# Kernel tuning notes

Measured on AMD Instinct MI355X. Metric: run time of the kernel, lower is better.

The kernel has to match this reference:

```python
import jax, jax.numpy as jnp
import numpy as np


def _procrustes_align(X, Y):
    """Batched similarity-transform (scipy-style Procrustes, reflection allowed).
    Aligns Y (pred) to X (target). X, Y: [B, N, 3]. Returns aligned Y: [B, N, 3].
    """
    muX = X.mean(axis=1, keepdims=True)                      # [B,1,3]
    muY = Y.mean(axis=1, keepdims=True)
    X0 = X - muX
    Y0 = Y - muY
    normX = jnp.sqrt((X0 ** 2).sum(axis=(1, 2), keepdims=True))  # [B,1,1]
    normY = jnp.sqrt((Y0 ** 2).sum(axis=(1, 2), keepdims=True))
    X0n = X0 / normX
    Y0n = Y0 / normY
    # 3x3 cross-covariance per batch element
    M = jnp.einsum('bni,bnj->bij', X0n, Y0n)                 # [B,3,3]
    U, s, Vt = jnp.linalg.svd(M)                             # batched tiny SVD
    # Optimal rotation Q = V @ U^T = (U @ Vt)^T  (minimizes ||Y0n @ Q - X0n||)
    Q = jnp.swapaxes(jnp.matmul(U, Vt), -1, -2)              # [B,3,3]
    traceTA = s.sum(-1)[:, None, None]                       # [B,1,1]
    Z = normX * traceTA * jnp.einsum('bni,bij->bnj', Y0n, Q) + muX
    return Z


def setup_inputs() -> dict:
    key = jax.random.key(0)
    k1, k2 = jax.random.split(key)
    B, N = 262144, 21
    pred_kp3d = jax.random.normal(k1, (B, N, 3), dtype=jnp.float32)
    target_kp3d = jax.random.normal(k2, (B, N, 3), dtype=jnp.float32)
    return {"pred_kp3d": pred_kp3d, "target_kp3d": target_kp3d}


def reference(pred_kp3d, target_kp3d):
    pred_aligned = _procrustes_align(target_kp3d, pred_kp3d)
    # mean per-joint Euclidean distance (PA-MPJPE style)
    err = jnp.sqrt(((pred_aligned - target_kp3d) ** 2).sum(-1)).mean()
    return err
```

## Files before the change

### kernel.cpp

```cpp
#include <hip/hip_runtime.h>
#include <math.h>

#define NPTS 21
#define FLB  63

__global__ __launch_bounds__(64, 2)
void pa_mpjpe(const float* __restrict__ pred,
              const float* __restrict__ targ,
              float* __restrict__ ws,
              int B)
{
    const int b = blockIdx.x * 64 + threadIdx.x;
    float errsum = 0.0f;

    if (b < B) {
        const float* gp = pred + (size_t)b * FLB;
        const float* gt = targ + (size_t)b * FLB;

        float yv[FLB];
        float xv[FLB];
        #pragma unroll
        for (int i = 0; i < 15; ++i) __builtin_memcpy(&yv[4*i], gp + 4*i, 16);
        __builtin_memcpy(&yv[60], gp + 60, 12);
        #pragma unroll
        for (int i = 0; i < 15; ++i) __builtin_memcpy(&xv[4*i], gt + 4*i, 16);
        __builtin_memcpy(&xv[60], gt + 60, 12);

        float sy0 = 0.f, sy1 = 0.f, sy2 = 0.f, syy = 0.f;
        #pragma unroll
        for (int n = 0; n < NPTS; ++n) {
            float a = yv[3*n+0], bb = yv[3*n+1], d = yv[3*n+2];
            sy0 += a; sy1 += bb; sy2 += d;
            syy = fmaf(a, a, fmaf(bb, bb, fmaf(d, d, syy)));
        }

        float sx0 = 0.f, sx1 = 0.f, sx2 = 0.f;
        float m00=0,m01=0,m02=0, m10=0,m11=0,m12=0, m20=0,m21=0,m22=0;
        #pragma unroll
        for (int n = 0; n < NPTS; ++n) {
            float a = xv[3*n+0], bb = xv[3*n+1], d = xv[3*n+2];
            float u = yv[3*n+0], v = yv[3*n+1], w = yv[3*n+2];
            sx0 += a; sx1 += bb; sx2 += d;
            m00 = fmaf(a,u,m00); m01 = fmaf(a,v,m01); m02 = fmaf(a,w,m02);
            m10 = fmaf(bb,u,m10); m11 = fmaf(bb,v,m11); m12 = fmaf(bb,w,m12);
            m20 = fmaf(d,u,m20); m21 = fmaf(d,v,m21); m22 = fmaf(d,w,m22);
        }

        const float invN = 1.0f / (float)NPTS;
        float mux0 = sx0*invN, mux1 = sx1*invN, mux2 = sx2*invN;
        float muy0 = sy0*invN, muy1 = sy1*invN, muy2 = sy2*invN;
        float ny2  = syy - (sy0*sy0 + sy1*sy1 + sy2*sy2) * invN;
        float c00 = m00 - sx0*sy0*invN, c01 = m01 - sx0*sy1*invN, c02 = m02 - sx0*sy2*invN;
        float c10 = m10 - sx1*sy0*invN, c11 = m11 - sx1*sy1*invN, c12 = m12 - sx1*sy2*invN;
        float c20 = m20 - sx2*sy0*invN, c21 = m21 - sx2*sy1*invN, c22 = m22 - sx2*sy2*invN;

        float q00=c00, q01=c10, q02=c20,
              q10=c01, q11=c11, q12=c21,
              q20=c02, q21=c12, q22=c22;
        #pragma unroll
        for (int it = 0; it < 8; ++it) {
            float C00 = q11*q22 - q12*q21;
            float C01 = q12*q20 - q10*q22;
            float C02 = q10*q21 - q11*q20;
            float C10 = q02*q21 - q01*q22;
            float C11 = q00*q22 - q02*q20;
            float C12 = q01*q20 - q00*q21;
            float C20 = q01*q12 - q02*q11;
            float C21 = q02*q10 - q00*q12;
            float C22 = q00*q11 - q01*q10;
            float det = q00*C00 + q01*C01 + q02*C02;
            float ad  = fmaxf(fabsf(det), 1e-30f);
            float sdet = copysignf(ad, det);
            float g  = __expf(0.333333333f * __logf(ad));
            float ha = 0.5f / g;
            float hb = 0.5f * g / sdet;
            q00 = ha*q00 + hb*C00; q01 = ha*q01 + hb*C01; q02 = ha*q02 + hb*C02;
            q10 = ha*q10 + hb*C10; q11 = ha*q11 + hb*C11; q12 = ha*q12 + hb*C12;
            q20 = ha*q20 + hb*C20; q21 = ha*q21 + hb*C21; q22 = ha*q22 + hb*C22;
        }

        float trP = q00*c00 + q01*c10 + q02*c20
                  + q10*c01 + q11*c11 + q12*c21
                  + q20*c02 + q21*c12 + q22*c22;
        float k = trP / ny2;
        float r00=k*q00, r01=k*q01, r02=k*q02;
        float r10=k*q10, r11=k*q11, r12=k*q12;
        float r20=k*q20, r21=k*q21, r22=k*q22;

        #pragma unroll
        for (int n = 0; n < NPTS; ++n) {
            float xa = xv[3*n+0], xb = xv[3*n+1], xc = xv[3*n+2];
            float u = yv[3*n+0] - muy0, v = yv[3*n+1] - muy1, w = yv[3*n+2] - muy2;
            float z0 = fmaf(u, r00, fmaf(v, r10, fmaf(w, r20, mux0))) - xa;
            float z1 = fmaf(u, r01, fmaf(v, r11, fmaf(w, r21, mux1))) - xb;
            float z2 = fmaf(u, r02, fmaf(v, r12, fmaf(w, r22, mux2))) - xc;
            errsum += sqrtf(fmaf(z0, z0, fmaf(z1, z1, z2*z2)));
        }
    }

    #pragma unroll
    for (int off = 32; off > 0; off >>= 1) errsum += __shfl_down(errsum, off, 64);
    if (threadIdx.x == 0) ws[blockIdx.x] = errsum;
}

__global__ __launch_bounds__(256)
void pa_reduce(const float* __restrict__ ws, float* __restrict__ out,
               int nblk, float inv_total)
{
    __shared__ float sw[4];
    float s = 0.0f;
    for (int i = threadIdx.x; i < nblk; i += 256) s += ws[i];
    #pragma unroll
    for (int off = 32; off > 0; off >>= 1) s += __shfl_down(s, off, 64);
    if ((threadIdx.x & 63) == 0) sw[threadIdx.x >> 6] = s;
    __syncthreads();
    if (threadIdx.x == 0)
        out[0] = (sw[0] + sw[1] + sw[2] + sw[3]) * inv_total;
}

extern "C" void kernel_launch(void* const* d_in, const int* in_sizes, int n_in,
                              void* d_out, int out_size, void* d_ws, size_t ws_size,
                              hipStream_t stream)
{
    const float* pred = (const float*)d_in[0];
    const float* targ = (const float*)d_in[1];
    float* out = (float*)d_out;
    float* ws  = (float*)d_ws;

    int B = in_sizes[0] / FLB;
    int grid = (B + 63) / 64;
    float inv_total = 1.0f / ((float)B * (float)NPTS);

    pa_mpjpe<<<grid, 64, 0, stream>>>(pred, targ, ws, B);
    pa_reduce<<<1, 256, 0, stream>>>(ws, out, grid, inv_total);
}
```

Baseline: 159.9 us.

## Stage batch chunks through LDS with async loads and split keypoints across lane pairs

Result: faster. 153.1 us (-4.2%).

```diff
diff --git a/kernel.cpp b/kernel.cpp
--- a/kernel.cpp
+++ b/kernel.cpp
@@ -3,104 +3,162 @@
 
 #define NPTS 21
 #define FLB  63
+#define BPB  32
+#define THREADS 64
+#define KPL  11
+#define CHUNK_FLOATS (BPB * FLB)
+#define NV4 (CHUNK_FLOATS / 4)
+#define FULL_ROUNDS (NV4 / THREADS)
+#define TAIL_LANES  (NV4 % THREADS)
 
-__global__ __launch_bounds__(64, 2)
+typedef __attribute__((address_space(3))) float       lds_f;
+typedef __attribute__((address_space(3))) void        lds_v;
+typedef const __attribute__((address_space(1))) void  gbl_v;
+
+__device__ __forceinline__ void async_cp16(const float* g, lds_f* l) {
+    __builtin_amdgcn_global_load_lds((gbl_v*)g, (lds_v*)l, 16, 0, 0);
+}
+
+__device__ __forceinline__ void stage_chunk(const float* gbase, lds_f* lbuf, int tid) {
+    #pragma unroll
+    for (int j = 0; j < FULL_ROUNDS; ++j)
+        async_cp16(gbase + 4 * (j * THREADS + tid), lbuf + 4 * (j * THREADS));
+    if (tid < TAIL_LANES)
+        async_cp16(gbase + 4 * (FULL_ROUNDS * THREADS + tid),
+                   lbuf + 4 * (FULL_ROUNDS * THREADS));
+}
+
+__global__ __launch_bounds__(THREADS, 4)
 void pa_mpjpe(const float* __restrict__ pred,
               const float* __restrict__ targ,
               float* __restrict__ ws,
-              int B)
+              int nchunk)
 {
-    const int b = blockIdx.x * 64 + threadIdx.x;
+    __shared__ __align__(16) float sb_[CHUNK_FLOATS];
+    lds_f* sb = (lds_f*)sb_;
+
+    const int tid = threadIdx.x;
+    const int lb  = tid >> 1;
+    const int h   = tid & 1;
+    const int base = lb * FLB;
+    const int c = blockIdx.x;
+
+    const float* gp = pred + (size_t)c * CHUNK_FLOATS;
+    const float* gt = targ + (size_t)c * CHUNK_FLOATS;
+
+    stage_chunk(gp, sb, tid);
+    asm volatile("s_waitcnt vmcnt(0)" ::: "memory");
+    __syncthreads();
+
+    float y[KPL][3];
+    float sy0 = 0.f, sy1 = 0.f, sy2 = 0.f, syy = 0.f;
+    #pragma unroll
+    for (int k = 0; k < KPL; ++k) {
+        int   n  = h * KPL + k;
+        float m  = (n < NPTS) ? 1.0f : 0.0f;
+        int   nn = (n < NPTS) ? n : (NPTS - 1);
+        float a = sb[base + 3*nn + 0] * m;
+        float b = sb[base + 3*nn + 1] * m;
+        float d = sb[base + 3*nn + 2] * m;
+        y[k][0] = a; y[k][1] = b; y[k][2] = d;
+        sy0 += a; sy1 += b; sy2 += d;
+        syy = fmaf(a, a, fmaf(b, b, fmaf(d, d, syy)));
+    }
+    sy0 += __shfl_xor(sy0, 1, 64);
+    sy1 += __shfl_xor(sy1, 1, 64);
+    sy2 += __shfl_xor(sy2, 1, 64);
+    syy += __shfl_xor(syy, 1, 64);
+
+    asm volatile("s_waitcnt lgkmcnt(0)" ::: "memory");
+    __syncthreads();
+
+    stage_chunk(gt, sb, tid);
+    asm volatile("s_waitcnt vmcnt(0)" ::: "memory");
+    __syncthreads();
+
+    float sx0 = 0.f, sx1 = 0.f, sx2 = 0.f;
+    float m00=0,m01=0,m02=0, m10=0,m11=0,m12=0, m20=0,m21=0,m22=0;
+    #pragma unroll
+    for (int k = 0; k < KPL; ++k) {
+        int   n  = h * KPL + k;
+        float m  = (n < NPTS) ? 1.0f : 0.0f;
+        int   nn = (n < NPTS) ? n : (NPTS - 1);
+        float a = sb[base + 3*nn + 0] * m;
+        float b = sb[base + 3*nn + 1] * m;
+        float d = sb[base + 3*nn + 2] * m;
+        float u = y[k][0], v = y[k][1], w = y[k][2];
+        sx0 += a; sx1 += b; sx2 += d;
+        m00 = fmaf(a,u,m00); m01 = fmaf(a,v,m01); m02 = fmaf(a,w,m02);
+        m10 = fmaf(b,u,m10); m11 = fmaf(b,v,m11); m12 = fmaf(b,w,m12);
+        m20 = fmaf(d,u,m20); m21 = fmaf(d,v,m21); m22 = fmaf(d,w,m22);
+    }
+    sx0 += __shfl_xor(sx0, 1, 64);
+    sx1 += __shfl_xor(sx1, 1, 64);
+    sx2 += __shfl_xor(sx2, 1, 64);
+    m00 += __shfl_xor(m00, 1, 64);  m01 += __shfl_xor(m01, 1, 64);  m02 += __shfl_xor(m02, 1, 64);
+    m10 += __shfl_xor(m10, 1, 64);  m11 += __shfl_xor(m11, 1, 64);  m12 += __shfl_xor(m12, 1, 64);
+    m20 += __shfl_xor(m20, 1, 64);  m21 += __shfl_xor(m21, 1, 64);  m22 += __shfl_xor(m22, 1, 64);
+
+    const float invN = 1.0f / (float)NPTS;
+    float mux0 = sx0*invN, mux1 = sx1*invN, mux2 = sx2*invN;
+    float muy0 = sy0*invN, muy1 = sy1*invN, muy2 = sy2*invN;
+    float ny2  = syy - (sy0*sy0 + sy1*sy1 + sy2*sy2) * invN;
+    float c00 = m00 - sx0*sy0*invN, c01 = m01 - sx0*sy1*invN, c02 = m02 - sx0*sy2*invN;
+    float c10 = m10 - sx1*sy0*invN, c11 = m11 - sx1*sy1*invN, c12 = m12 - sx1*sy2*invN;
+    float c20 = m20 - sx2*sy0*invN, c21 = m21 - sx2*sy1*invN, c22 = m22 - sx2*sy2*invN;
+
+    float q00=c00, q01=c10, q02=c20,
+          q10=c01, q11=c11, q12=c21,
+          q20=c02, q21=c12, q22=c22;
+    #pragma unroll
+    for (int it = 0; it < 8; ++it) {
+        float C00 = q11*q22 - q12*q21;
+        float C01 = q12*q20 - q10*q22;
+        float C02 = q10*q21 - q11*q20;
+        float C10 = q02*q21 - q01*q22;
+        float C11 = q00*q22 - q02*q20;
+        float C12 = q01*q20 - q00*q21;
+        float C20 = q01*q12 - q02*q11;
+        float C21 = q02*q10 - q00*q12;
+        float C22 = q00*q11 - q01*q10;
+        float det = q00*C00 + q01*C01 + q02*C02;
+        float ad  = fmaxf(fabsf(det), 1e-30f);
+        float sdet = copysignf(ad, det);
+        float g  = __expf(0.333333333f * __logf(ad));
+        float ha = 0.5f / g;
+        float hb = 0.5f * g / sdet;
+        q00 = ha*q00 + hb*C00; q01 = ha*q01 + hb*C01; q02 = ha*q02 + hb*C02;
+        q10 = ha*q10 + hb*C10; q11 = ha*q11 + hb*C11; q12 = ha*q12 + hb*C12;
+        q20 = ha*q20 + hb*C20; q21 = ha*q21 + hb*C21; q22 = ha*q22 + hb*C22;
+    }
+
+    float trP = q00*c00 + q01*c10 + q02*c20
+              + q10*c01 + q11*c11 + q12*c21
+              + q20*c02 + q21*c12 + q22*c22;
+    float kk = trP / ny2;
+    float r00=kk*q00, r01=kk*q01, r02=kk*q02;
+    float r10=kk*q10, r11=kk*q11, r12=kk*q12;
+    float r20=kk*q20, r21=kk*q21, r22=kk*q22;
+
     float errsum = 0.0f;
-
-    if (b < B) {
-        const float* gp = pred + (size_t)b * FLB;
-        const float* gt = targ + (size_t)b * FLB;
-
-        float yv[FLB];
-        float xv[FLB];
-        #pragma unroll
-        for (int i = 0; i < 15; ++i) __builtin_memcpy(&yv[4*i], gp + 4*i, 16);
-        __builtin_memcpy(&yv[60], gp + 60, 12);
-        #pragma unroll
-        for (int i = 0; i < 15; ++i) __builtin_memcpy(&xv[4*i], gt + 4*i, 16);
-        __builtin_memcpy(&xv[60], gt + 60, 12);
-
-        float sy0 = 0.f, sy1 = 0.f, sy2 = 0.f, syy = 0.f;
-        #pragma unroll
-        for (int n = 0; n < NPTS; ++n) {
-            float a = yv[3*n+0], bb = yv[3*n+1], d = yv[3*n+2];
-            sy0 += a; sy1 += bb; sy2 += d;
-            syy = fmaf(a, a, fmaf(bb, bb, fmaf(d, d, syy)));
-        }
-
-        float sx0 = 0.f, sx1 = 0.f, sx2 = 0.f;
-        float m00=0,m01=0,m02=0, m10=0,m11=0,m12=0, m20=0,m21=0,m22=0;
-        #pragma unroll
-        for (int n = 0; n < NPTS; ++n) {
-            float a = xv[3*n+0], bb = xv[3*n+1], d = xv[3*n+2];
-            float u = yv[3*n+0], v = yv[3*n+1], w = yv[3*n+2];
-            sx0 += a; sx1 += bb; sx2 += d;
-            m00 = fmaf(a,u,m00); m01 = fmaf(a,v,m01); m02 = fmaf(a,w,m02);
-            m10 = fmaf(bb,u,m10); m11 = fmaf(bb,v,m11); m12 = fmaf(bb,w,m12);
-            m20 = fmaf(d,u,m20); m21 = fmaf(d,v,m21); m22 = fmaf(d,w,m22);
-        }
-
-        const float invN = 1.0f / (float)NPTS;
-        float mux0 = sx0*invN, mux1 = sx1*invN, mux2 = sx2*invN;
-        float muy0 = sy0*invN, muy1 = sy1*invN, muy2 = sy2*invN;
-        float ny2  = syy - (sy0*sy0 + sy1*sy1 + sy2*sy2) * invN;
-        float c00 = m00 - sx0*sy0*invN, c01 = m01 - sx0*sy1*invN, c02 = m02 - sx0*sy2*invN;
-        float c10 = m10 - sx1*sy0*invN, c11 = m11 - sx1*sy1*invN, c12 = m12 - sx1*sy2*invN;
-        float c20 = m20 - sx2*sy0*invN, c21 = m21 - sx2*sy1*invN, c22 = m22 - sx2*sy2*invN;
-
-        float q00=c00, q01=c10, q02=c20,
-              q10=c01, q11=c11, q12=c21,
-              q20=c02, q21=c12, q22=c22;
-        #pragma unroll
-        for (int it = 0; it < 8; ++it) {
-            float C00 = q11*q22 - q12*q21;
-            float C01 = q12*q20 - q10*q22;
-            float C02 = q10*q21 - q11*q20;
-            float C10 = q02*q21 - q01*q22;
-            float C11 = q00*q22 - q02*q20;
-            float C12 = q01*q20 - q00*q21;
-            float C20 = q01*q12 - q02*q11;
-            float C21 = q02*q10 - q00*q12;
-            float C22 = q00*q11 - q01*q10;
-            float det = q00*C00 + q01*C01 + q02*C02;
-            float ad  = fmaxf(fabsf(det), 1e-30f);
-            float sdet = copysignf(ad, det);
-            float g  = __expf(0.333333333f * __logf(ad));
-            float ha = 0.5f / g;
-            float hb = 0.5f * g / sdet;
-            q00 = ha*q00 + hb*C00; q01 = ha*q01 + hb*C01; q02 = ha*q02 + hb*C02;
-            q10 = ha*q10 + hb*C10; q11 = ha*q11 + hb*C11; q12 = ha*q12 + hb*C12;
-            q20 = ha*q20 + hb*C20; q21 = ha*q21 + hb*C21; q22 = ha*q22 + hb*C22;
-        }
-
-        float trP = q00*c00 + q01*c10 + q02*c20
-                  + q10*c01 + q11*c11 + q12*c21
-                  + q20*c02 + q21*c12 + q22*c22;
-        float k = trP / ny2;
-        float r00=k*q00, r01=k*q01, r02=k*q02;
-        float r10=k*q10, r11=k*q11, r12=k*q12;
-        float r20=k*q20, r21=k*q21, r22=k*q22;
-
-        #pragma unroll
-        for (int n = 0; n < NPTS; ++n) {
-            float xa = xv[3*n+0], xb = xv[3*n+1], xc = xv[3*n+2];
-            float u = yv[3*n+0] - muy0, v = yv[3*n+1] - muy1, w = yv[3*n+2] - muy2;
-            float z0 = fmaf(u, r00, fmaf(v, r10, fmaf(w, r20, mux0))) - xa;
-            float z1 = fmaf(u, r01, fmaf(v, r11, fmaf(w, r21, mux1))) - xb;
-            float z2 = fmaf(u, r02, fmaf(v, r12, fmaf(w, r22, mux2))) - xc;
-            errsum += sqrtf(fmaf(z0, z0, fmaf(z1, z1, z2*z2)));
-        }
+    #pragma unroll
+    for (int k = 0; k < KPL; ++k) {
+        int   n  = h * KPL + k;
+        float m  = (n < NPTS) ? 1.0f : 0.0f;
+        int   nn = (n < NPTS) ? n : (NPTS - 1);
+        float xa = sb[base + 3*nn + 0];
+        float xb = sb[base + 3*nn + 1];
+        float xc = sb[base + 3*nn + 2];
+        float u = y[k][0] - muy0, v = y[k][1] - muy1, w = y[k][2] - muy2;
+        float z0 = fmaf(u, r00, fmaf(v, r10, fmaf(w, r20, mux0))) - xa;
+        float z1 = fmaf(u, r01, fmaf(v, r11, fmaf(w, r21, mux1))) - xb;
+        float z2 = fmaf(u, r02, fmaf(v, r12, fmaf(w, r22, mux2))) - xc;
+        errsum += m * sqrtf(fmaf(z0, z0, fmaf(z1, z1, z2*z2)));
     }
 
     #pragma unroll
     for (int off = 32; off > 0; off >>= 1) errsum += __shfl_down(errsum, off, 64);
-    if (threadIdx.x == 0) ws[blockIdx.x] = errsum;
+    if (tid == 0) ws[blockIdx.x] = errsum;
 }
 
 __global__ __launch_bounds__(256)
@@ -128,9 +186,9 @@
     float* ws  = (float*)d_ws;
 
     int B = in_sizes[0] / FLB;
-    int grid = (B + 63) / 64;
+    int nchunk = B / BPB;
     float inv_total = 1.0f / ((float)B * (float)NPTS);
 
-    pa_mpjpe<<<grid, 64, 0, stream>>>(pred, targ, ws, B);
-    pa_reduce<<<1, 256, 0, stream>>>(ws, out, grid, inv_total);
+    pa_mpjpe<<<nchunk, THREADS, 0, stream>>>(pred, targ, ws, nchunk);
+    pa_reduce<<<1, 256, 0, stream>>>(ws, out, nchunk, inv_total);
 }
```
